# Kernel tuning notes

Hardware: AMD Instinct MI355X
Metric: run time of the kernel (lower is better)

The kernel has to match this reference:

```python
import jax, jax.numpy as jnp
import numpy as np

N, E, B, T, H, L = 8192, 2048, 512, 128, 128, 3


def setup_inputs() -> dict:
    key = jax.random.key(0)
    ks = jax.random.split(key, 14)
    # sparse binary hyperedge incidence [E, N]
    Hbat = (jax.random.uniform(ks[0], (E, N)) < 0.01).astype(jnp.float32)
    DV2 = jax.random.uniform(ks[1], (N,)) + 0.1    # D_v^{-1/2} node scaling
    invDE = jax.random.uniform(ks[2], (E,)) + 0.1  # D_e^{-1} edge scaling
    data = jax.random.randint(ks[3], (B, T), 0, N, dtype=jnp.int32)
    lens = jax.random.randint(ks[4], (B,), 1, T + 1, dtype=jnp.int32)
    data_length = jnp.sort(lens)[::-1].at[0].set(T)  # descending, max == T (pack_padded)
    poi = jax.random.normal(ks[5], (N, H), dtype=jnp.float32)
    s = 1.0 / float(np.sqrt(H))
    hgc1_w = jax.random.uniform(ks[6], (H, H), minval=-s, maxval=s)
    hgc1_b = jax.random.uniform(ks[7], (H,), minval=-s, maxval=s)
    hgc2_w = jax.random.uniform(ks[8], (H, H), minval=-s, maxval=s)
    hgc2_b = jax.random.uniform(ks[9], (H,), minval=-s, maxval=s)
    Wih = jax.random.uniform(ks[10], (L, 3 * H, H), minval=-s, maxval=s)
    Whh = jax.random.uniform(ks[11], (L, 3 * H, H), minval=-s, maxval=s)
    bih = jax.random.uniform(ks[12], (L, 3 * H), minval=-s, maxval=s)
    bhh = jax.random.uniform(ks[13], (L, 3 * H), minval=-s, maxval=s)
    return dict(Hbat=Hbat, DV2=DV2, invDE=invDE, data=data, data_length=data_length,
                poi=poi, hgc1_w=hgc1_w, hgc1_b=hgc1_b, hgc2_w=hgc2_w, hgc2_b=hgc2_b,
                Wih=Wih, Whh=Whh, bih=bih, bhh=bhh)


def _gru(x, Wih, Whh, bih, bhh):
    # torch nn.GRU (batch_first, 1 layer, h0=0). x: [B,T,H] -> [B,T,H]
    gx = jnp.einsum('bth,gh->btg', x, Wih) + bih  # precompute input gates [B,T,3H]

    def step(h, gxt):
        gh = h @ Whh.T + bhh
        xr, xz, xn = jnp.split(gxt, 3, axis=-1)
        hr, hz, hn = jnp.split(gh, 3, axis=-1)
        r = jax.nn.sigmoid(xr + hr)
        z = jax.nn.sigmoid(xz + hz)
        n = jnp.tanh(xn + r * hn)
        h_new = (1.0 - z) * n + z * h
        return h_new, h_new

    h0 = jnp.zeros((x.shape[0], x.shape[2]), x.dtype)
    _, ys = jax.lax.scan(step, h0, jnp.swapaxes(gx, 0, 1))
    return jnp.swapaxes(ys, 0, 1)


def reference(Hbat, DV2, invDE, data, data_length, poi,
              hgc1_w, hgc1_b, hgc2_w, hgc2_b, Wih, Whh, bih, bhh):
    # G = diag(DV2) Hbat^T diag(invDE) Hbat diag(DV2); diag_embed GEMMs == row/col scaling
    G = (DV2[:, None] * Hbat.T) @ (invDE[:, None] * Hbat * DV2[None, :])  # [N,N]
    x = jax.nn.relu(G @ (poi @ hgc1_w + hgc1_b)) + poi
    x = G @ (x @ hgc2_w + hgc2_b)
    batch_emb = x[data]  # [B,T,H]
    Tn = batch_emb.shape[1]
    # pad_packed_sequence zero-fills beyond each sequence's length
    mask = (jnp.arange(Tn)[None, :] < data_length[:, None])[:, :, None].astype(batch_emb.dtype)
    inp = batch_emb
    n_layers = Wih.shape[0]
    for l in range(n_layers - 1):
        out = _gru(inp, Wih[l], Whh[l], bih[l], bhh[l]) * mask
        inp = batch_emb + jax.nn.relu(out)
    out = _gru(inp, Wih[-1], Whh[-1], bih[-1], bhh[-1]) * mask
    last = out[jnp.arange(out.shape[0]), data_length - 1]  # gather last valid step
    return jnp.tanh(last)
```

## Files before the change

### kernel.cpp

```cpp
#include <hip/hip_runtime.h>

#define NN 8192
#define EE 2048
#define BB 512
#define TT 128
#define HH 128
#define G3 384
#define MAXNNZ 256
#define MAXDEG 96

typedef __attribute__((ext_vector_type(8))) _Float16 f16x8;
typedef __attribute__((ext_vector_type(4))) float f32x4;

__device__ __forceinline__ float sigm(float x){ return 1.0f/(1.0f+__expf(-x)); }
__device__ __forceinline__ float tanhfast(float x){ return 2.0f/(1.0f+__expf(-2.0f*x)) - 1.0f; }

__device__ __forceinline__ void bar_lds(){
  __builtin_amdgcn_sched_barrier(0);
  asm volatile("s_waitcnt lgkmcnt(0)\n\ts_barrier" ::: "memory");
  __builtin_amdgcn_sched_barrier(0);
}

__global__ __launch_bounds__(256)
void build_nnz(const float* __restrict__ Hb, int* __restrict__ idx, int* __restrict__ cnt){
  __shared__ int c;
  const int e = blockIdx.x;
  if (threadIdx.x == 0) c = 0;
  __syncthreads();
  const float* row = Hb + (size_t)e * NN;
  for (int n = threadIdx.x; n < NN; n += 256){
    if (row[n] != 0.0f){
      int p = atomicAdd(&c, 1);
      if (p < MAXNNZ) idx[e*MAXNNZ + p] = n;
    }
  }
  __syncthreads();
  if (threadIdx.x == 0) cnt[e] = (c < MAXNNZ ? c : MAXNNZ);
}

__global__ __launch_bounds__(128)
void build_nodelists(const int* __restrict__ idx, const int* __restrict__ cnt,
                     int* __restrict__ ndeg, int* __restrict__ nidx){
  const int e = blockIdx.x;
  const int c = cnt[e];
  for (int k = threadIdx.x; k < c; k += 128){
    int n = idx[e*MAXNNZ + k];
    int p = atomicAdd(&ndeg[n], 1);
    if (p < MAXDEG) nidx[n*MAXDEG + p] = e;
  }
}

__global__ __launch_bounds__(256)
void prep_w(const float* __restrict__ W, _Float16* __restrict__ whi,
            _Float16* __restrict__ wlo, int n){
  int i = blockIdx.x*256 + threadIdx.x;
  if (i >= n) return;
  float g = W[i] * 16.0f;
  _Float16 h = (_Float16)g;
  whi[i] = h;
  wlo[i] = (_Float16)(g - (float)h);
}

__global__ __launch_bounds__(256)
void prep_split(const float* __restrict__ X, _Float16* __restrict__ hi,
                _Float16* __restrict__ lo, int n){
  int i = blockIdx.x*256 + threadIdx.x;
  if (i >= n) return;
  float v = X[i];
  _Float16 h = (_Float16)v;
  hi[i] = h;
  lo[i] = (_Float16)(v - (float)h);
}

__global__ __launch_bounds__(256)
void prep_wt(const float* __restrict__ W, _Float16* __restrict__ wt_hi,
             _Float16* __restrict__ wt_lo){
  int i = blockIdx.x*256 + threadIdx.x;
  int k = i >> 7, j = i & 127;
  float g = W[i] * 16.0f;
  _Float16 h = (_Float16)g;
  wt_hi[j*HH + k] = h;
  wt_lo[j*HH + k] = (_Float16)(g - (float)h);
}

template<bool SCALE>
__global__ __launch_bounds__(256)
void mm128_mfma(const _Float16* __restrict__ Ahi, const _Float16* __restrict__ Alo,
                const _Float16* __restrict__ Bh, const _Float16* __restrict__ Bl,
                const float* __restrict__ bias, const float* __restrict__ rowscale,
                float* __restrict__ C)
{
  const int tid = threadIdx.x;
  const int w = tid >> 6, l = tid & 63;
  const int lm = l & 15, q = l >> 4;
  const int r0 = blockIdx.x * 32;
  const int n0 = w * 32;

  f32x4 acc[2][2];
  #pragma unroll
  for (int m=0;m<2;m++)
    #pragma unroll
    for (int n=0;n<2;n++) acc[m][n] = (f32x4){0.f,0.f,0.f,0.f};

  #pragma unroll 2
  for (int ks = 0; ks < 4; ++ks){
    const int kb = ks*32 + q*8;
    f16x8 ah[2], al[2];
    #pragma unroll
    for (int m=0;m<2;m++){
      const size_t ro = (size_t)(r0 + m*16 + lm)*HH + kb;
      ah[m] = *(const f16x8*)(Ahi + ro);
      al[m] = *(const f16x8*)(Alo + ro);
    }
    #pragma unroll
    for (int n=0;n<2;n++){
      const int j = n0 + n*16 + lm;
      f16x8 bh = *(const f16x8*)(Bh + (size_t)j*HH + kb);
      f16x8 bl = *(const f16x8*)(Bl + (size_t)j*HH + kb);
      #pragma unroll
      for (int m=0;m<2;m++){
        acc[m][n] = __builtin_amdgcn_mfma_f32_16x16x32_f16(ah[m], bh, acc[m][n], 0,0,0);
        acc[m][n] = __builtin_amdgcn_mfma_f32_16x16x32_f16(al[m], bh, acc[m][n], 0,0,0);
        acc[m][n] = __builtin_amdgcn_mfma_f32_16x16x32_f16(ah[m], bl, acc[m][n], 0,0,0);
      }
    }
  }
  #pragma unroll
  for (int n=0;n<2;n++){
    const int j = n0 + n*16 + lm;
    const float bv = bias[j];
    #pragma unroll
    for (int m=0;m<2;m++){
      #pragma unroll
      for (int i=0;i<4;i++){
        int r = r0 + m*16 + q*4 + i;
        float cv = acc[m][n][i]*(1.0f/16.0f) + bv;
        if (SCALE) cv *= rowscale[r];
        C[(size_t)r*HH + j] = cv;
      }
    }
  }
}

__global__ __launch_bounds__(128)
void edge_gather(const float* __restrict__ Xs, const int* __restrict__ idx,
                 const int* __restrict__ cnt, const float* __restrict__ invDE,
                 float* __restrict__ Eb){
  __shared__ int sidx[MAXNNZ];
  const int e = blockIdx.x, h = threadIdx.x;
  const int c = cnt[e];
  for (int k = h; k < c; k += 128) sidx[k] = idx[e*MAXNNZ + k];
  __syncthreads();
  float acc = 0.0f;
  int k = 0;
  for (; k + 4 <= c; k += 4){
    float a0 = Xs[(size_t)sidx[k+0]*HH + h];
    float a1 = Xs[(size_t)sidx[k+1]*HH + h];
    float a2 = Xs[(size_t)sidx[k+2]*HH + h];
    float a3 = Xs[(size_t)sidx[k+3]*HH + h];
    acc += (a0 + a1) + (a2 + a3);
  }
  for (; k < c; ++k) acc += Xs[(size_t)sidx[k]*HH + h];
  Eb[e*HH + h] = invDE[e] * acc;
}

template<int MODE>
__global__ __launch_bounds__(128)
void node_gather(const float* __restrict__ Eb, const int* __restrict__ nidx,
                 const int* __restrict__ ndeg, const float* __restrict__ DV2,
                 const float* __restrict__ poi, _Float16* __restrict__ ohi,
                 _Float16* __restrict__ olo, float* __restrict__ Xo){
  __shared__ int sidx[MAXDEG];
  const int n = blockIdx.x, h = threadIdx.x;
  int c = ndeg[n]; c = c < MAXDEG ? c : MAXDEG;
  for (int k = h; k < c; k += 128) sidx[k] = nidx[n*MAXDEG + k];
  __syncthreads();
  float acc = 0.0f;
  int k = 0;
  for (; k + 4 <= c; k += 4){
    float a0 = Eb[(size_t)sidx[k+0]*HH + h];
    float a1 = Eb[(size_t)sidx[k+1]*HH + h];
    float a2 = Eb[(size_t)sidx[k+2]*HH + h];
    float a3 = Eb[(size_t)sidx[k+3]*HH + h];
    acc += (a0 + a1) + (a2 + a3);
  }
  for (; k < c; ++k) acc += Eb[(size_t)sidx[k]*HH + h];
  float v = DV2[n] * acc;
  if (MODE == 1){
    float val = fmaxf(v, 0.0f) + poi[(size_t)n*HH + h];
    _Float16 hh = (_Float16)val;
    ohi[(size_t)n*HH + h] = hh;
    olo[(size_t)n*HH + h] = (_Float16)(val - (float)hh);
  } else {
    Xo[(size_t)n*HH + h] = v;
  }
}

__global__ __launch_bounds__(256)
void gather_emb(const float* __restrict__ X, const int* __restrict__ data,
                float* __restrict__ emb, _Float16* __restrict__ aHi,
                _Float16* __restrict__ aLo){
  int r = blockIdx.x*2 + (threadIdx.x >> 7);
  int h = threadIdx.x & 127;
  int n = data[r];
  float v = X[(size_t)n*HH + h];
  size_t o = (size_t)r*HH + h;
  emb[o] = v;
  _Float16 hh = (_Float16)v;
  aHi[o] = hh;
  aLo[o] = (_Float16)(v - (float)hh);
}

__global__ __launch_bounds__(512, 1)
void gru_fused(const float* __restrict__ WhhAll, const float* __restrict__ bhhAll,
               const _Float16* __restrict__ WhiAll, const _Float16* __restrict__ WloAll,
               const float* __restrict__ bihAll, const int* __restrict__ lens,
               const float* __restrict__ emb, _Float16* __restrict__ aHi,
               _Float16* __restrict__ aLo, float* __restrict__ gxb,
               float* __restrict__ out)
{
  __shared__ _Float16 hbuf[2][16*HH];
  __shared__ float ghT[2][392];
  const int tid = threadIdx.x;
  const int w = tid >> 6, lane = tid & 63;
  const int lm = lane & 15, q = lane >> 4;
  const int b0 = blockIdx.x * 2;
  const int n0 = w * 48;

  const int len0 = lens[b0], len1 = lens[b0+1];
  const int lenmax = len0;
  const int ntl[2] = {(len0+15)>>4, (len1+15)>>4};

  const int gb = (tid < 256) ? (tid >> 7) : 0;
  const int gd = tid & 127;
  const float* gxrow = gxb + (size_t)(b0+gb)*TT*G3;
  const float* erow  = emb + (size_t)(b0+gb)*TT*HH + gd;
  _Float16* ahrow = aHi + (size_t)(b0+gb)*TT*HH + gd;
  _Float16* alrow = aLo + (size_t)(b0+gb)*TT*HH + gd;
  const int glen = gb ? len1 : len0;

  #pragma unroll 1
  for (int l = 0; l < 3; ++l){
    const bool fin = (l == 2);
    const _Float16* Whi = WhiAll + (size_t)l*G3*HH;
    const _Float16* Wlo = WloAll + (size_t)l*G3*HH;
    const float* bih = bihAll + l*G3;
    const float* Whh = WhhAll + (size_t)l*G3*HH;
    const float* bhh = bhhAll + l*G3;

    #pragma unroll 1
    for (int bb = 0; bb < 2; ++bb){
      const int ntb = ntl[bb];
      #pragma unroll 1
      for (int rt = 0; rt < ntb; ++rt){
        f32x4 acc0 = (f32x4){0.f,0.f,0.f,0.f}, acc1 = acc0, acc2 = acc0;
        #pragma unroll
        for (int ks = 0; ks < 4; ++ks){
          const int kb = ks*32 + q*8;
          const size_t ro = ((size_t)(b0+bb)*TT + rt*16 + lm)*HH + kb;
          f16x8 ah = *(const f16x8*)(aHi + ro);
          f16x8 al = *(const f16x8*)(aLo + ro);
          {
            const int g = n0 + lm;
            f16x8 bh = *(const f16x8*)(Whi + (size_t)g*HH + kb);
            f16x8 bl = *(const f16x8*)(Wlo + (size_t)g*HH + kb);
            acc0 = __builtin_amdgcn_mfma_f32_16x16x32_f16(ah, bh, acc0, 0,0,0);
            acc0 = __builtin_amdgcn_mfma_f32_16x16x32_f16(al, bh, acc0, 0,0,0);
            acc0 = __builtin_amdgcn_mfma_f32_16x16x32_f16(ah, bl, acc0, 0,0,0);
          }
          {
            const int g = n0 + 16 + lm;
            f16x8 bh = *(const f16x8*)(Whi + (size_t)g*HH + kb);
            f16x8 bl = *(const f16x8*)(Wlo + (size_t)g*HH + kb);
            acc1 = __builtin_amdgcn_mfma_f32_16x16x32_f16(ah, bh, acc1, 0,0,0);
            acc1 = __builtin_amdgcn_mfma_f32_16x16x32_f16(al, bh, acc1, 0,0,0);
            acc1 = __builtin_amdgcn_mfma_f32_16x16x32_f16(ah, bl, acc1, 0,0,0);
          }
          {
            const int g = n0 + 32 + lm;
            f16x8 bh = *(const f16x8*)(Whi + (size_t)g*HH + kb);
            f16x8 bl = *(const f16x8*)(Wlo + (size_t)g*HH + kb);
            acc2 = __builtin_amdgcn_mfma_f32_16x16x32_f16(ah, bh, acc2, 0,0,0);
            acc2 = __builtin_amdgcn_mfma_f32_16x16x32_f16(al, bh, acc2, 0,0,0);
            acc2 = __builtin_amdgcn_mfma_f32_16x16x32_f16(ah, bl, acc2, 0,0,0);
          }
        }
        float* gout = gxb + ((size_t)(b0+bb)*TT + rt*16)*G3;
        #pragma unroll
        for (int i=0;i<4;i++){
          const int t = q*4 + i;
          gout[(size_t)t*G3 + n0 + lm]      = acc0[i]*(1.0f/16.0f) + bih[n0 + lm];
          gout[(size_t)t*G3 + n0 + 16 + lm] = acc1[i]*(1.0f/16.0f) + bih[n0 + 16 + lm];
          gout[(size_t)t*G3 + n0 + 32 + lm] = acc2[i]*(1.0f/16.0f) + bih[n0 + 32 + lm];
        }
      }
    }

    f16x8 wf[3][4];
    #pragma unroll
    for (int n=0; n<3; ++n){
      const int col = n0 + n*16 + lm;
      const float* wr = Whh + (size_t)col*HH;
      #pragma unroll
      for (int ks=0; ks<4; ++ks){
        const int kb = ks*32 + q*8;
        float4 f0 = *(const float4*)(wr + kb);
        float4 f1 = *(const float4*)(wr + kb + 4);
        float fv[8] = {f0.x,f0.y,f0.z,f0.w,f1.x,f1.y,f1.z,f1.w};
        union { f16x8 v; _Float16 u[8]; } uu;
        #pragma unroll
        for (int j=0;j<8;j++) uu.u[j] = (_Float16)(fv[j] * 16.0f);
        wf[n][ks] = uu.v;
      }
    }
    const float S = 1.0f/16.0f;
    const float bR = bhh[gd], bZ = bhh[HH+gd], bN = bhh[2*HH+gd];

    {
      unsigned int* z = (unsigned int*)&hbuf[0][0];
      #pragma unroll 1
      for (int i = tid; i < 2*16*HH/2; i += 512) z[i] = 0u;
    }
    __syncthreads();

    float xv0=0.f, xv1=0.f, xv2=0.f, xe=0.f, hp=0.f, fo=0.f;
    if (tid < 256){
      xv0 = gxrow[gd]; xv1 = gxrow[128+gd]; xv2 = gxrow[256+gd];
      if (!fin) xe = erow[0];
    }

    int cur = 0;
    #pragma unroll 1
    for (int t = 0; t < lenmax; ++t){
      f16x8 av[4];
      #pragma unroll
      for (int ks=0; ks<4; ++ks){
        int off = (lm*256 + ks*64 + q*16) ^ ((lm & 7) << 4);
        av[ks] = *(const f16x8*)((const char*)&hbuf[cur][0] + off);
      }
      float xn0=0.f, xn1=0.f, xn2=0.f, xen=0.f;
      if (tid < 256){
        int tp = (t+1 < lenmax) ? t+1 : t;
        const float* bgx = gxrow + (size_t)tp*G3;
        xn0 = bgx[gd]; xn1 = bgx[128+gd]; xn2 = bgx[256+gd];
        if (!fin) xen = erow[(size_t)tp*HH];
      }
      f32x4 a0 = (f32x4){0.f,0.f,0.f,0.f}, a1 = a0, a2 = a0;
      #pragma unroll
      for (int ks=0; ks<4; ++ks){
        a0 = __builtin_amdgcn_mfma_f32_16x16x32_f16(av[ks], wf[0][ks], a0, 0,0,0);
        a1 = __builtin_amdgcn_mfma_f32_16x16x32_f16(av[ks], wf[1][ks], a1, 0,0,0);
        a2 = __builtin_amdgcn_mfma_f32_16x16x32_f16(av[ks], wf[2][ks], a2, 0,0,0);
      }
      if (q == 0){
        const int c0 = n0 + lm;
        ghT[0][c0]      = a0[0];  ghT[1][c0]      = a0[1];
        ghT[0][c0+16]   = a1[0];  ghT[1][c0+16]   = a1[1];
        ghT[0][c0+32]   = a2[0];  ghT[1][c0+32]   = a2[1];
      }
      bar_lds();

      if (tid < 256){
        float gr = ghT[gb][gd], gz = ghT[gb][128+gd], gn = ghT[gb][256+gd];
        float r = sigm(xv0 + gr*S + bR);
        float z = sigm(xv1 + gz*S + bZ);
        float n = tanhfast(xv2 + r*(gn*S + bN));
        float hnew = (1.0f - z)*n + z*hp;
        hp = hnew;
        int off = (gb*256 + gd*2) ^ (gb << 4);
        *(_Float16*)((char*)&hbuf[cur^1][0] + off) = (_Float16)hnew;
        if (!fin){
          float a = xe + fmaxf(hnew, 0.0f);
          _Float16 ah = (_Float16)a;
          ahrow[(size_t)t*HH] = ah;
          alrow[(size_t)t*HH] = (_Float16)(a - (float)ah);
        } else {
          if (t == glen - 1) fo = tanhfast(hnew);
        }
      }
      xv0 = xn0; xv1 = xn1; xv2 = xn2; xe = xen;
      bar_lds();
      cur ^= 1;
    }

    if (fin){
      if (tid < 256)
        out[(size_t)(b0+gb)*HH + gd] = fo;
    } else {
      __syncthreads();
    }
  }
}

extern "C" void kernel_launch(void* const* d_in, const int* in_sizes, int n_in,
                              void* d_out, int out_size, void* d_ws, size_t ws_size,
                              hipStream_t stream)
{
  const float* Hb    = (const float*)d_in[0];
  const float* DV2   = (const float*)d_in[1];
  const float* invDE = (const float*)d_in[2];
  const int*   data  = (const int*)d_in[3];
  const int*   dlen  = (const int*)d_in[4];
  const float* poi   = (const float*)d_in[5];
  const float* w1    = (const float*)d_in[6];
  const float* b1    = (const float*)d_in[7];
  const float* w2    = (const float*)d_in[8];
  const float* b2    = (const float*)d_in[9];
  const float* Wih   = (const float*)d_in[10];
  const float* Whh   = (const float*)d_in[11];
  const float* bih   = (const float*)d_in[12];
  const float* bhh   = (const float*)d_in[13];
  float* out = (float*)d_out;

  float* ws   = (float*)d_ws;
  float* x1s  = ws;
  float* x3s  = x1s + (size_t)NN*HH;
  float* x4   = x3s + (size_t)NN*HH;
  float* ebuf = x4  + (size_t)NN*HH;
  float* gx   = ebuf + (size_t)EE*HH;
  float* emb  = gx  + (size_t)BB*TT*G3;
  _Float16* aHi  = (_Float16*)(emb + (size_t)BB*TT*HH);
  _Float16* aLo  = aHi + (size_t)BB*TT*HH;
  _Float16* x2hi = aLo + (size_t)BB*TT*HH;
  _Float16* x2lo = x2hi + (size_t)NN*HH;
  _Float16* pHi  = x2lo + (size_t)NN*HH;
  _Float16* pLo  = pHi + (size_t)NN*HH;
  _Float16* Whi  = pLo + (size_t)NN*HH;
  _Float16* Wlo  = Whi + (size_t)3*G3*HH;
  _Float16* w1th = Wlo + (size_t)3*G3*HH;
  _Float16* w1tl = w1th + (size_t)HH*HH;
  _Float16* w2th = w1tl + (size_t)HH*HH;
  _Float16* w2tl = w2th + (size_t)HH*HH;
  int* idx  = (int*)(w2tl + (size_t)HH*HH);
  int* cnt  = idx + (size_t)EE*MAXNNZ;
  int* ndeg = cnt + EE;
  int* nidx = ndeg + NN;

  hipMemsetAsync(ndeg, 0, NN*sizeof(int), stream);
  build_nnz<<<EE, 256, 0, stream>>>(Hb, idx, cnt);
  build_nodelists<<<EE, 128, 0, stream>>>(idx, cnt, ndeg, nidx);
  prep_w<<<(3*G3*HH + 255)/256, 256, 0, stream>>>(Wih, Whi, Wlo, 3*G3*HH);
  prep_wt<<<HH*HH/256, 256, 0, stream>>>(w1, w1th, w1tl);
  prep_wt<<<HH*HH/256, 256, 0, stream>>>(w2, w2th, w2tl);
  prep_split<<<NN*HH/256, 256, 0, stream>>>(poi, pHi, pLo, NN*HH);

  mm128_mfma<true><<<NN/32, 256, 0, stream>>>(pHi, pLo, w1th, w1tl, b1, DV2, x1s);
  edge_gather<<<EE, 128, 0, stream>>>(x1s, idx, cnt, invDE, ebuf);
  node_gather<1><<<NN, 128, 0, stream>>>(ebuf, nidx, ndeg, DV2, poi, x2hi, x2lo, (float*)nullptr);
  mm128_mfma<true><<<NN/32, 256, 0, stream>>>(x2hi, x2lo, w2th, w2tl, b2, DV2, x3s);
  edge_gather<<<EE, 128, 0, stream>>>(x3s, idx, cnt, invDE, ebuf);
  node_gather<2><<<NN, 128, 0, stream>>>(ebuf, nidx, ndeg, DV2, (const float*)nullptr,
                                         (_Float16*)nullptr, (_Float16*)nullptr, x4);
  gather_emb<<<BB*TT/2, 256, 0, stream>>>(x4, data, emb, aHi, aLo);

  gru_fused<<<BB/2, 512, 0, stream>>>(Whh, bhh, Whi, Wlo, bih, dlen,
                                      emb, aHi, aLo, gx, out);
}
```

Before: 495.2 us.

## Overlap input-gate GEMM with GRU recurrence via LDS ring buffer

Input-gate projections are no longer computed for the whole sequence up front and written to global gx. Each 16-step chunk is now computed during the previous chunk's recurrent steps and stored in a double-buffered shared-memory ring, with the GEMM loads and MFMAs interleaved across alternating timesteps. The float emb copy is dropped and the skip input is rebuilt from the hi/lo fp16 split. Separate ping-pong activation buffers avoid overwriting a layer's input while it is read. The cost is about 98KB of extra LDS and more register pressure in the serial loop.

```diff
diff --git a/kernel.cpp b/kernel.cpp
--- a/kernel.cpp
+++ b/kernel.cpp
@@ -198,29 +198,30 @@
 
 __global__ __launch_bounds__(256)
 void gather_emb(const float* __restrict__ X, const int* __restrict__ data,
-                float* __restrict__ emb, _Float16* __restrict__ aHi,
-                _Float16* __restrict__ aLo){
+                _Float16* __restrict__ aHi, _Float16* __restrict__ aLo){
   int r = blockIdx.x*2 + (threadIdx.x >> 7);
   int h = threadIdx.x & 127;
   int n = data[r];
   float v = X[(size_t)n*HH + h];
   size_t o = (size_t)r*HH + h;
-  emb[o] = v;
   _Float16 hh = (_Float16)v;
   aHi[o] = hh;
   aLo[o] = (_Float16)(v - (float)hh);
 }
 
 __global__ __launch_bounds__(512, 1)
-void gru_fused(const float* __restrict__ WhhAll, const float* __restrict__ bhhAll,
-               const _Float16* __restrict__ WhiAll, const _Float16* __restrict__ WloAll,
-               const float* __restrict__ bihAll, const int* __restrict__ lens,
-               const float* __restrict__ emb, _Float16* __restrict__ aHi,
-               _Float16* __restrict__ aLo, float* __restrict__ gxb,
-               float* __restrict__ out)
+void gru_fused2(const float* __restrict__ WhhAll, const float* __restrict__ bhhAll,
+                const _Float16* __restrict__ WhiAll, const _Float16* __restrict__ WloAll,
+                const float* __restrict__ bihAll, const int* __restrict__ lens,
+                const _Float16* __restrict__ a0Hi, const _Float16* __restrict__ a0Lo,
+                _Float16* __restrict__ aAHi, _Float16* __restrict__ aALo,
+                _Float16* __restrict__ aBHi, _Float16* __restrict__ aBLo,
+                float* __restrict__ out)
 {
   __shared__ _Float16 hbuf[2][16*HH];
   __shared__ float ghT[2][392];
+  __shared__ float ring[2][2][16][G3];
+
   const int tid = threadIdx.x;
   const int w = tid >> 6, lane = tid & 63;
   const int lm = lane & 15, q = lane >> 4;
@@ -229,15 +230,14 @@
 
   const int len0 = lens[b0], len1 = lens[b0+1];
   const int lenmax = len0;
-  const int ntl[2] = {(len0+15)>>4, (len1+15)>>4};
+  const int nch = (lenmax + 15) >> 4;
 
   const int gb = (tid < 256) ? (tid >> 7) : 0;
   const int gd = tid & 127;
-  const float* gxrow = gxb + (size_t)(b0+gb)*TT*G3;
-  const float* erow  = emb + (size_t)(b0+gb)*TT*HH + gd;
-  _Float16* ahrow = aHi + (size_t)(b0+gb)*TT*HH + gd;
-  _Float16* alrow = aLo + (size_t)(b0+gb)*TT*HH + gd;
   const int glen = gb ? len1 : len0;
+  const size_t eb = ((size_t)(b0+gb)*TT)*HH + gd;
+
+  const float S = 1.0f/16.0f;
 
   #pragma unroll 1
   for (int l = 0; l < 3; ++l){
@@ -247,60 +247,17 @@
     const float* bih = bihAll + l*G3;
     const float* Whh = WhhAll + (size_t)l*G3*HH;
     const float* bhh = bhhAll + l*G3;
-
-    #pragma unroll 1
-    for (int bb = 0; bb < 2; ++bb){
-      const int ntb = ntl[bb];
-      #pragma unroll 1
-      for (int rt = 0; rt < ntb; ++rt){
-        f32x4 acc0 = (f32x4){0.f,0.f,0.f,0.f}, acc1 = acc0, acc2 = acc0;
-        #pragma unroll
-        for (int ks = 0; ks < 4; ++ks){
-          const int kb = ks*32 + q*8;
-          const size_t ro = ((size_t)(b0+bb)*TT + rt*16 + lm)*HH + kb;
-          f16x8 ah = *(const f16x8*)(aHi + ro);
-          f16x8 al = *(const f16x8*)(aLo + ro);
-          {
-            const int g = n0 + lm;
-            f16x8 bh = *(const f16x8*)(Whi + (size_t)g*HH + kb);
-            f16x8 bl = *(const f16x8*)(Wlo + (size_t)g*HH + kb);
-            acc0 = __builtin_amdgcn_mfma_f32_16x16x32_f16(ah, bh, acc0, 0,0,0);
-            acc0 = __builtin_amdgcn_mfma_f32_16x16x32_f16(al, bh, acc0, 0,0,0);
-            acc0 = __builtin_amdgcn_mfma_f32_16x16x32_f16(ah, bl, acc0, 0,0,0);
-          }
-          {
-            const int g = n0 + 16 + lm;
-            f16x8 bh = *(const f16x8*)(Whi + (size_t)g*HH + kb);
-            f16x8 bl = *(const f16x8*)(Wlo + (size_t)g*HH + kb);
-            acc1 = __builtin_amdgcn_mfma_f32_16x16x32_f16(ah, bh, acc1, 0,0,0);
-            acc1 = __builtin_amdgcn_mfma_f32_16x16x32_f16(al, bh, acc1, 0,0,0);
-            acc1 = __builtin_amdgcn_mfma_f32_16x16x32_f16(ah, bl, acc1, 0,0,0);
-          }
-          {
-            const int g = n0 + 32 + lm;
-            f16x8 bh = *(const f16x8*)(Whi + (size_t)g*HH + kb);
-            f16x8 bl = *(const f16x8*)(Wlo + (size_t)g*HH + kb);
-            acc2 = __builtin_amdgcn_mfma_f32_16x16x32_f16(ah, bh, acc2, 0,0,0);
-            acc2 = __builtin_amdgcn_mfma_f32_16x16x32_f16(al, bh, acc2, 0,0,0);
-            acc2 = __builtin_amdgcn_mfma_f32_16x16x32_f16(ah, bl, acc2, 0,0,0);
-          }
-        }
-        float* gout = gxb + ((size_t)(b0+bb)*TT + rt*16)*G3;
-        #pragma unroll
-        for (int i=0;i<4;i++){
-          const int t = q*4 + i;
-          gout[(size_t)t*G3 + n0 + lm]      = acc0[i]*(1.0f/16.0f) + bih[n0 + lm];
-          gout[(size_t)t*G3 + n0 + 16 + lm] = acc1[i]*(1.0f/16.0f) + bih[n0 + 16 + lm];
-          gout[(size_t)t*G3 + n0 + 32 + lm] = acc2[i]*(1.0f/16.0f) + bih[n0 + 32 + lm];
-        }
-      }
-    }
+    const _Float16* aInHi = (l==0) ? a0Hi : (l==1 ? aAHi : aBHi);
+    const _Float16* aInLo = (l==0) ? a0Lo : (l==1 ? aALo : aBLo);
+    _Float16* aOutHi = (l==0) ? aAHi : aBHi;
+    _Float16* aOutLo = (l==0) ? aALo : aBLo;
+
+    const float bv0 = bih[n0+lm], bv1 = bih[n0+16+lm], bv2 = bih[n0+32+lm];
 
     f16x8 wf[3][4];
     #pragma unroll
     for (int n=0; n<3; ++n){
-      const int col = n0 + n*16 + lm;
-      const float* wr = Whh + (size_t)col*HH;
+      const float* wr = Whh + (size_t)(n0 + n*16 + lm)*HH;
       #pragma unroll
       for (int ks=0; ks<4; ++ks){
         const int kb = ks*32 + q*8;
@@ -313,50 +270,105 @@
         wf[n][ks] = uu.v;
       }
     }
-    const float S = 1.0f/16.0f;
     const float bR = bhh[gd], bZ = bhh[HH+gd], bN = bhh[2*HH+gd];
+
+    f16x8 gah, gal, gb0h, gb0l, gb1h, gb1l, gb2h, gb2l;
+    f32x4 ag0 = (f32x4){0.f,0.f,0.f,0.f}, ag1 = ag0, ag2 = ag0;
+
+    auto GXLOAD = [&](int chn2, int p){
+      const int bb = p >> 2, ks = p & 3, kb = ks*32 + q*8;
+      const size_t ro = ((size_t)(b0+bb)*TT + chn2*16 + lm)*HH + kb;
+      gah = *(const f16x8*)(aInHi + ro);
+      gal = *(const f16x8*)(aInLo + ro);
+      const size_t wb = (size_t)(n0+lm)*HH + kb;
+      gb0h = *(const f16x8*)(Whi + wb);
+      gb0l = *(const f16x8*)(Wlo + wb);
+      gb1h = *(const f16x8*)(Whi + wb + (size_t)16*HH);
+      gb1l = *(const f16x8*)(Wlo + wb + (size_t)16*HH);
+      gb2h = *(const f16x8*)(Whi + wb + (size_t)32*HH);
+      gb2l = *(const f16x8*)(Wlo + wb + (size_t)32*HH);
+    };
+    auto GXMFMA = [&](){
+      ag0 = __builtin_amdgcn_mfma_f32_16x16x32_f16(gah, gb0h, ag0, 0,0,0);
+      ag0 = __builtin_amdgcn_mfma_f32_16x16x32_f16(gal, gb0h, ag0, 0,0,0);
+      ag0 = __builtin_amdgcn_mfma_f32_16x16x32_f16(gah, gb0l, ag0, 0,0,0);
+      ag1 = __builtin_amdgcn_mfma_f32_16x16x32_f16(gah, gb1h, ag1, 0,0,0);
+      ag1 = __builtin_amdgcn_mfma_f32_16x16x32_f16(gal, gb1h, ag1, 0,0,0);
+      ag1 = __builtin_amdgcn_mfma_f32_16x16x32_f16(gah, gb1l, ag1, 0,0,0);
+      ag2 = __builtin_amdgcn_mfma_f32_16x16x32_f16(gah, gb2h, ag2, 0,0,0);
+      ag2 = __builtin_amdgcn_mfma_f32_16x16x32_f16(gal, gb2h, ag2, 0,0,0);
+      ag2 = __builtin_amdgcn_mfma_f32_16x16x32_f16(gah, gb2l, ag2, 0,0,0);
+    };
+    auto GXWRITE = [&](int chn2, int bb){
+      #pragma unroll
+      for (int i=0;i<4;i++){
+        ring[chn2&1][bb][q*4+i][n0+lm]      = ag0[i]*S + bv0;
+        ring[chn2&1][bb][q*4+i][n0+16+lm]   = ag1[i]*S + bv1;
+        ring[chn2&1][bb][q*4+i][n0+32+lm]   = ag2[i]*S + bv2;
+      }
+      ag0 = (f32x4){0.f,0.f,0.f,0.f}; ag1 = ag0; ag2 = ag0;
+    };
 
     {
       unsigned int* z = (unsigned int*)&hbuf[0][0];
       #pragma unroll 1
       for (int i = tid; i < 2*16*HH/2; i += 512) z[i] = 0u;
     }
+
+    #pragma unroll 1
+    for (int p = 0; p < 8; ++p){
+      GXLOAD(0, p);
+      GXMFMA();
+      if (p == 3) GXWRITE(0, 0);
+      if (p == 7) GXWRITE(0, 1);
+    }
     __syncthreads();
 
-    float xv0=0.f, xv1=0.f, xv2=0.f, xe=0.f, hp=0.f, fo=0.f;
-    if (tid < 256){
-      xv0 = gxrow[gd]; xv1 = gxrow[128+gd]; xv2 = gxrow[256+gd];
-      if (!fin) xe = erow[0];
-    }
+    float xe = 0.f, hp = 0.f, fo = 0.f;
+    if (tid < 256 && !fin)
+      xe = (float)a0Hi[eb] + (float)a0Lo[eb];
 
     int cur = 0;
     #pragma unroll 1
     for (int t = 0; t < lenmax; ++t){
+      const int s = t & 15;
+      const int chn = (t >> 4) + 1;
+      const bool doGx = chn < nch;
+
       f16x8 av[4];
       #pragma unroll
       for (int ks=0; ks<4; ++ks){
         int off = (lm*256 + ks*64 + q*16) ^ ((lm & 7) << 4);
         av[ks] = *(const f16x8*)((const char*)&hbuf[cur][0] + off);
       }
-      float xn0=0.f, xn1=0.f, xn2=0.f, xen=0.f;
+      float xv0=0.f, xv1=0.f, xv2=0.f, xen=0.f;
       if (tid < 256){
-        int tp = (t+1 < lenmax) ? t+1 : t;
-        const float* bgx = gxrow + (size_t)tp*G3;
-        xn0 = bgx[gd]; xn1 = bgx[128+gd]; xn2 = bgx[256+gd];
-        if (!fin) xen = erow[(size_t)tp*HH];
-      }
-      f32x4 a0 = (f32x4){0.f,0.f,0.f,0.f}, a1 = a0, a2 = a0;
+        const float* rp = &ring[(t>>4)&1][gb][s][0];
+        xv0 = rp[gd]; xv1 = rp[128+gd]; xv2 = rp[256+gd];
+        if (!fin){
+          int tp = (t+1 < lenmax) ? t+1 : t;
+          xen = (float)a0Hi[eb + (size_t)tp*HH] + (float)a0Lo[eb + (size_t)tp*HH];
+        }
+      }
+      if (doGx && !(s & 1)) GXLOAD(chn, s >> 1);
+
+      f32x4 aGH0 = (f32x4){0.f,0.f,0.f,0.f}, aGH1 = aGH0, aGH2 = aGH0;
       #pragma unroll
       for (int ks=0; ks<4; ++ks){
-        a0 = __builtin_amdgcn_mfma_f32_16x16x32_f16(av[ks], wf[0][ks], a0, 0,0,0);
-        a1 = __builtin_amdgcn_mfma_f32_16x16x32_f16(av[ks], wf[1][ks], a1, 0,0,0);
-        a2 = __builtin_amdgcn_mfma_f32_16x16x32_f16(av[ks], wf[2][ks], a2, 0,0,0);
+        aGH0 = __builtin_amdgcn_mfma_f32_16x16x32_f16(av[ks], wf[0][ks], aGH0, 0,0,0);
+        aGH1 = __builtin_amdgcn_mfma_f32_16x16x32_f16(av[ks], wf[1][ks], aGH1, 0,0,0);
+        aGH2 = __builtin_amdgcn_mfma_f32_16x16x32_f16(av[ks], wf[2][ks], aGH2, 0,0,0);
+      }
+      if (doGx && (s & 1)){
+        GXMFMA();
+        if (s == 7)  GXWRITE(chn, 0);
+        else if (s == 15) GXWRITE(chn, 1);
       }
       if (q == 0){
         const int c0 = n0 + lm;
-        ghT[0][c0]      = a0[0];  ghT[1][c0]      = a0[1];
-        ghT[0][c0+16]   = a1[0];  ghT[1][c0+16]   = a1[1];
-        ghT[0][c0+32]   = a2[0];  ghT[1][c0+32]   = a2[1];
+        ghT[0][c0]      = aGH0[0];  ghT[1][c0]      = aGH0[1];
+        ghT[0][c0+16]   = aGH1[0];  ghT[1][c0+16]   = aGH1[1];
+        ghT[0][c0+32]   = aGH2[0];  ghT[1][c0+32]   = aGH2[1];
       }
       bar_lds();
 
@@ -372,13 +384,13 @@
         if (!fin){
           float a = xe + fmaxf(hnew, 0.0f);
           _Float16 ah = (_Float16)a;
-          ahrow[(size_t)t*HH] = ah;
-          alrow[(size_t)t*HH] = (_Float16)(a - (float)ah);
+          aOutHi[eb + (size_t)t*HH] = ah;
+          aOutLo[eb + (size_t)t*HH] = (_Float16)(a - (float)ah);
         } else {
           if (t == glen - 1) fo = tanhfast(hnew);
         }
       }
-      xv0 = xn0; xv1 = xn1; xv2 = xn2; xe = xen;
+      xe = xen;
       bar_lds();
       cur ^= 1;
     }
@@ -417,11 +429,13 @@
   float* x3s  = x1s + (size_t)NN*HH;
   float* x4   = x3s + (size_t)NN*HH;
   float* ebuf = x4  + (size_t)NN*HH;
-  float* gx   = ebuf + (size_t)EE*HH;
-  float* emb  = gx  + (size_t)BB*TT*G3;
-  _Float16* aHi  = (_Float16*)(emb + (size_t)BB*TT*HH);
-  _Float16* aLo  = aHi + (size_t)BB*TT*HH;
-  _Float16* x2hi = aLo + (size_t)BB*TT*HH;
+  _Float16* a0Hi = (_Float16*)(ebuf + (size_t)EE*HH);
+  _Float16* a0Lo = a0Hi + (size_t)BB*TT*HH;
+  _Float16* aAHi = a0Lo + (size_t)BB*TT*HH;
+  _Float16* aALo = aAHi + (size_t)BB*TT*HH;
+  _Float16* aBHi = aALo + (size_t)BB*TT*HH;
+  _Float16* aBLo = aBHi + (size_t)BB*TT*HH;
+  _Float16* x2hi = aBLo + (size_t)BB*TT*HH;
   _Float16* x2lo = x2hi + (size_t)NN*HH;
   _Float16* pHi  = x2lo + (size_t)NN*HH;
   _Float16* pLo  = pHi + (size_t)NN*HH;
@@ -451,8 +465,8 @@
   edge_gather<<<EE, 128, 0, stream>>>(x3s, idx, cnt, invDE, ebuf);
   node_gather<2><<<NN, 128, 0, stream>>>(ebuf, nidx, ndeg, DV2, (const float*)nullptr,
                                          (_Float16*)nullptr, (_Float16*)nullptr, x4);
-  gather_emb<<<BB*TT/2, 256, 0, stream>>>(x4, data, emb, aHi, aLo);
-
-  gru_fused<<<BB/2, 512, 0, stream>>>(Whh, bhh, Whi, Wlo, bih, dlen,
-                                      emb, aHi, aLo, gx, out);
-}
+  gather_emb<<<BB*TT/2, 256, 0, stream>>>(x4, data, a0Hi, a0Lo);
+
+  gru_fused2<<<BB/2, 512, 0, stream>>>(Whh, bhh, Whi, Wlo, bih, dlen,
+                                       a0Hi, a0Lo, aAHi, aALo, aBHi, aBLo, out);
+}
```

Result: slower. 645.4 us (+30.3%).

## Drop fp32 emb buffer, ping-pong GRU activations, swizzle blocks, split MFMA chains

Applied to the files above, without the earlier changes.

The fp32 embedding copy is removed. The GRU residual input is now rebuilt from the fp16 hi/lo split of layer 0, and each layer writes its input to separate ping-pong buffers instead of overwriting one in place. Block indices are swizzled so that blocks with different sequence lengths are interleaved across CUs, which should balance the length-dependent work. The recurrent MFMA chain is also split into two independent accumulators to shorten the dependency latency per step, and the input-projection loop is unrolled by 2. In exchange this uses more workspace and adds a small fp16-pair reconstruction cost on each residual read.

```diff
diff --git a/kernel.cpp b/kernel.cpp
--- a/kernel.cpp
+++ b/kernel.cpp
@@ -198,14 +198,12 @@
 
 __global__ __launch_bounds__(256)
 void gather_emb(const float* __restrict__ X, const int* __restrict__ data,
-                float* __restrict__ emb, _Float16* __restrict__ aHi,
-                _Float16* __restrict__ aLo){
+                _Float16* __restrict__ aHi, _Float16* __restrict__ aLo){
   int r = blockIdx.x*2 + (threadIdx.x >> 7);
   int h = threadIdx.x & 127;
   int n = data[r];
   float v = X[(size_t)n*HH + h];
   size_t o = (size_t)r*HH + h;
-  emb[o] = v;
   _Float16 hh = (_Float16)v;
   aHi[o] = hh;
   aLo[o] = (_Float16)(v - (float)hh);
@@ -215,8 +213,10 @@
 void gru_fused(const float* __restrict__ WhhAll, const float* __restrict__ bhhAll,
                const _Float16* __restrict__ WhiAll, const _Float16* __restrict__ WloAll,
                const float* __restrict__ bihAll, const int* __restrict__ lens,
-               const float* __restrict__ emb, _Float16* __restrict__ aHi,
-               _Float16* __restrict__ aLo, float* __restrict__ gxb,
+               const float* __restrict__ emb_unused, _Float16* __restrict__ a0Hi,
+               _Float16* __restrict__ a0Lo, _Float16* __restrict__ aAHi,
+               _Float16* __restrict__ aALo, _Float16* __restrict__ aBHi,
+               _Float16* __restrict__ aBLo, float* __restrict__ gxb,
                float* __restrict__ out)
 {
   __shared__ _Float16 hbuf[2][16*HH];
@@ -224,7 +224,9 @@
   const int tid = threadIdx.x;
   const int w = tid >> 6, lane = tid & 63;
   const int lm = lane & 15, q = lane >> 4;
-  const int b0 = blockIdx.x * 2;
+  const int p = blockIdx.x;
+  const int swz = ((p & 7) << 5) | (p >> 3);
+  const int b0 = swz * 2;
   const int n0 = w * 48;
 
   const int len0 = lens[b0], len1 = lens[b0+1];
@@ -234,10 +236,9 @@
   const int gb = (tid < 256) ? (tid >> 7) : 0;
   const int gd = tid & 127;
   const float* gxrow = gxb + (size_t)(b0+gb)*TT*G3;
-  const float* erow  = emb + (size_t)(b0+gb)*TT*HH + gd;
-  _Float16* ahrow = aHi + (size_t)(b0+gb)*TT*HH + gd;
-  _Float16* alrow = aLo + (size_t)(b0+gb)*TT*HH + gd;
+  _Float16* ahrow; _Float16* alrow;
   const int glen = gb ? len1 : len0;
+  const size_t eb = ((size_t)(b0+gb)*TT)*HH + gd;
 
   #pragma unroll 1
   for (int l = 0; l < 3; ++l){
@@ -247,19 +248,23 @@
     const float* bih = bihAll + l*G3;
     const float* Whh = WhhAll + (size_t)l*G3*HH;
     const float* bhh = bhhAll + l*G3;
+    const _Float16* aInHi = (l==0) ? a0Hi : (l==1 ? aAHi : aBHi);
+    const _Float16* aInLo = (l==0) ? a0Lo : (l==1 ? aALo : aBLo);
+    _Float16* aOutHi = (l==0) ? aAHi : aBHi;
+    _Float16* aOutLo = (l==0) ? aALo : aBLo;
 
     #pragma unroll 1
     for (int bb = 0; bb < 2; ++bb){
       const int ntb = ntl[bb];
-      #pragma unroll 1
+      #pragma unroll 2
       for (int rt = 0; rt < ntb; ++rt){
         f32x4 acc0 = (f32x4){0.f,0.f,0.f,0.f}, acc1 = acc0, acc2 = acc0;
         #pragma unroll
         for (int ks = 0; ks < 4; ++ks){
           const int kb = ks*32 + q*8;
           const size_t ro = ((size_t)(b0+bb)*TT + rt*16 + lm)*HH + kb;
-          f16x8 ah = *(const f16x8*)(aHi + ro);
-          f16x8 al = *(const f16x8*)(aLo + ro);
+          f16x8 ah = *(const f16x8*)(aInHi + ro);
+          f16x8 al = *(const f16x8*)(aInLo + ro);
           {
             const int g = n0 + lm;
             f16x8 bh = *(const f16x8*)(Whi + (size_t)g*HH + kb);
@@ -315,6 +320,8 @@
     }
     const float S = 1.0f/16.0f;
     const float bR = bhh[gd], bZ = bhh[HH+gd], bN = bhh[2*HH+gd];
+    ahrow = aOutHi + eb;
+    alrow = aOutLo + eb;
 
     {
       unsigned int* z = (unsigned int*)&hbuf[0][0];
@@ -326,7 +333,7 @@
     float xv0=0.f, xv1=0.f, xv2=0.f, xe=0.f, hp=0.f, fo=0.f;
     if (tid < 256){
       xv0 = gxrow[gd]; xv1 = gxrow[128+gd]; xv2 = gxrow[256+gd];
-      if (!fin) xe = erow[0];
+      if (!fin) xe = (float)a0Hi[eb] + (float)a0Lo[eb];
     }
 
     int cur = 0;
@@ -343,20 +350,27 @@
         int tp = (t+1 < lenmax) ? t+1 : t;
         const float* bgx = gxrow + (size_t)tp*G3;
         xn0 = bgx[gd]; xn1 = bgx[128+gd]; xn2 = bgx[256+gd];
-        if (!fin) xen = erow[(size_t)tp*HH];
-      }
-      f32x4 a0 = (f32x4){0.f,0.f,0.f,0.f}, a1 = a0, a2 = a0;
-      #pragma unroll
-      for (int ks=0; ks<4; ++ks){
-        a0 = __builtin_amdgcn_mfma_f32_16x16x32_f16(av[ks], wf[0][ks], a0, 0,0,0);
-        a1 = __builtin_amdgcn_mfma_f32_16x16x32_f16(av[ks], wf[1][ks], a1, 0,0,0);
-        a2 = __builtin_amdgcn_mfma_f32_16x16x32_f16(av[ks], wf[2][ks], a2, 0,0,0);
-      }
+        if (!fin) xen = (float)a0Hi[eb + (size_t)tp*HH] + (float)a0Lo[eb + (size_t)tp*HH];
+      }
+      f32x4 a0a = (f32x4){0.f,0.f,0.f,0.f}, a1a = a0a, a2a = a0a;
+      f32x4 a0b = a0a, a1b = a0a, a2b = a0a;
+      a0a = __builtin_amdgcn_mfma_f32_16x16x32_f16(av[0], wf[0][0], a0a, 0,0,0);
+      a1a = __builtin_amdgcn_mfma_f32_16x16x32_f16(av[0], wf[1][0], a1a, 0,0,0);
+      a2a = __builtin_amdgcn_mfma_f32_16x16x32_f16(av[0], wf[2][0], a2a, 0,0,0);
+      a0b = __builtin_amdgcn_mfma_f32_16x16x32_f16(av[2], wf[0][2], a0b, 0,0,0);
+      a1b = __builtin_amdgcn_mfma_f32_16x16x32_f16(av[2], wf[1][2], a1b, 0,0,0);
+      a2b = __builtin_amdgcn_mfma_f32_16x16x32_f16(av[2], wf[2][2], a2b, 0,0,0);
+      a0a = __builtin_amdgcn_mfma_f32_16x16x32_f16(av[1], wf[0][1], a0a, 0,0,0);
+      a1a = __builtin_amdgcn_mfma_f32_16x16x32_f16(av[1], wf[1][1], a1a, 0,0,0);
+      a2a = __builtin_amdgcn_mfma_f32_16x16x32_f16(av[1], wf[2][1], a2a, 0,0,0);
+      a0b = __builtin_amdgcn_mfma_f32_16x16x32_f16(av[3], wf[0][3], a0b, 0,0,0);
+      a1b = __builtin_amdgcn_mfma_f32_16x16x32_f16(av[3], wf[1][3], a1b, 0,0,0);
+      a2b = __builtin_amdgcn_mfma_f32_16x16x32_f16(av[3], wf[2][3], a2b, 0,0,0);
       if (q == 0){
         const int c0 = n0 + lm;
-        ghT[0][c0]      = a0[0];  ghT[1][c0]      = a0[1];
-        ghT[0][c0+16]   = a1[0];  ghT[1][c0+16]   = a1[1];
-        ghT[0][c0+32]   = a2[0];  ghT[1][c0+32]   = a2[1];
+        ghT[0][c0]      = a0a[0] + a0b[0];  ghT[1][c0]      = a0a[1] + a0b[1];
+        ghT[0][c0+16]   = a1a[0] + a1b[0];  ghT[1][c0+16]   = a1a[1] + a1b[1];
+        ghT[0][c0+32]   = a2a[0] + a2b[0];  ghT[1][c0+32]   = a2a[1] + a2b[1];
       }
       bar_lds();
 
@@ -418,10 +432,13 @@
   float* x4   = x3s + (size_t)NN*HH;
   float* ebuf = x4  + (size_t)NN*HH;
   float* gx   = ebuf + (size_t)EE*HH;
-  float* emb  = gx  + (size_t)BB*TT*G3;
-  _Float16* aHi  = (_Float16*)(emb + (size_t)BB*TT*HH);
-  _Float16* aLo  = aHi + (size_t)BB*TT*HH;
-  _Float16* x2hi = aLo + (size_t)BB*TT*HH;
+  _Float16* a0Hi = (_Float16*)(gx + (size_t)BB*TT*G3);
+  _Float16* a0Lo = a0Hi + (size_t)BB*TT*HH;
+  _Float16* aAHi = a0Lo + (size_t)BB*TT*HH;
+  _Float16* aALo = aAHi + (size_t)BB*TT*HH;
+  _Float16* aBHi = aALo + (size_t)BB*TT*HH;
+  _Float16* aBLo = aBHi + (size_t)BB*TT*HH;
+  _Float16* x2hi = aBLo + (size_t)BB*TT*HH;
   _Float16* x2lo = x2hi + (size_t)NN*HH;
   _Float16* pHi  = x2lo + (size_t)NN*HH;
   _Float16* pLo  = pHi + (size_t)NN*HH;
@@ -451,8 +468,9 @@
   edge_gather<<<EE, 128, 0, stream>>>(x3s, idx, cnt, invDE, ebuf);
   node_gather<2><<<NN, 128, 0, stream>>>(ebuf, nidx, ndeg, DV2, (const float*)nullptr,
                                          (_Float16*)nullptr, (_Float16*)nullptr, x4);
-  gather_emb<<<BB*TT/2, 256, 0, stream>>>(x4, data, emb, aHi, aLo);
+  gather_emb<<<BB*TT/2, 256, 0, stream>>>(x4, data, a0Hi, a0Lo);
 
   gru_fused<<<BB/2, 512, 0, stream>>>(Whh, bhh, Whi, Wlo, bih, dlen,
-                                      emb, aHi, aLo, gx, out);
-}
+                                      (const float*)nullptr, a0Hi, a0Lo,
+                                      aAHi, aALo, aBHi, aBLo, gx, out);
+}
```

Result: slower. 554.4 us (+11.9%).
